# Performance work log

Measured on AMD Instinct MI355X. Metric: run time of the kernel, lower is better.

The kernel has to match this reference:

```python
import jax, jax.numpy as jnp
import numpy as np

EDGE_TYPES = 5
D = 256      # input_dim == output_dim
HID = 128    # hard-coded hidden size of agg MLPs


def setup_inputs() -> dict:
    key = jax.random.key(0)
    ks = jax.random.split(key, 8)
    B, E, N = 4, 8000, 2000
    edge_distribution = jax.random.uniform(ks[0], (B, E, EDGE_TYPES), dtype=jnp.float32)
    H = jax.random.normal(ks[1], (B, E, N), dtype=jnp.float32)
    ori = jax.random.normal(ks[2], (B, N, D), dtype=jnp.float32)
    # Stacked per-edge-type MLP params: Linear(D->128), ReLU, Linear(128->D)
    W1 = jax.random.normal(ks[3], (EDGE_TYPES, D, HID), dtype=jnp.float32) * (1.0 / np.sqrt(D))
    b1 = jax.random.normal(ks[4], (EDGE_TYPES, HID), dtype=jnp.float32) * 0.01
    W2 = jax.random.normal(ks[5], (EDGE_TYPES, HID, D), dtype=jnp.float32) * (1.0 / np.sqrt(HID))
    b2 = jax.random.normal(ks[6], (EDGE_TYPES, D), dtype=jnp.float32) * 0.01
    return {"edge_distribution": edge_distribution, "H": H, "ori": ori,
            "W1": W1, "b1": b1, "W2": W2, "b2": b2}


def reference(edge_distribution, H, ori, W1, b1, W2, b2):
    # edges = H @ ori : [B, E, D]
    edges = jnp.matmul(H, ori)
    # Per-edge-type 2-layer MLP, vectorized over the type axis t
    h = jax.nn.relu(jnp.einsum('bed,tdh->tbeh', edges, W1) + b1[:, None, None, :])  # [T,B,E,HID]
    mlp_out = jnp.einsum('tbeh,thd->tbed', h, W2) + b2[:, None, None, :]            # [T,B,E,D]
    # Gated accumulate: sum_t edge_distribution[...,t] * mlp_out[t]
    edge_feature = jnp.einsum('bet,tbed->bed', edge_distribution, mlp_out)          # [B,E,D]
    # node_feature = concat(H^T @ edge_feature, ori)
    node_feature = jnp.concatenate(
        [jnp.matmul(jnp.swapaxes(H, 1, 2), edge_feature), ori], axis=-1)            # [B,N,2D]
    return node_feature
```

## Files before the change

### kernel.cpp

```cpp
#include <hip/hip_runtime.h>

typedef unsigned short u16;
typedef short bf16x8 __attribute__((ext_vector_type(8)));
typedef float f32x4 __attribute__((ext_vector_type(4)));
typedef unsigned short u16x8 __attribute__((ext_vector_type(8)));

#define GLL16(gp, lp) __builtin_amdgcn_global_load_lds( \
    (__attribute__((address_space(1))) const unsigned int*)(gp), \
    (__attribute__((address_space(3))) unsigned int*)(lp), 16, 0, 0)

static __device__ __forceinline__ u16 f2bf(float f){
  unsigned u = __builtin_bit_cast(unsigned, f);
  u += 0x7fffu + ((u >> 16) & 1u);
  return (u16)(u >> 16);
}

__global__ __launch_bounds__(256) void prep_ht(const float* __restrict__ H, u16* __restrict__ HT){
  __shared__ u16 t[64*68];
  const int b = blockIdx.z;
  const int e0 = blockIdx.x*64, n0 = blockIdx.y*64;
  const float* Hb = H + (size_t)b*8000*2000;
  u16* To = HT + (size_t)b*2048*8000;
  const int tid = threadIdx.x;
  const int cg = (tid&15)*4, rb = tid>>4;
  #pragma unroll
  for (int rr=0; rr<4; rr++){
    int row = rb + rr*16;
    int gn = n0 + cg;
    float4 v = make_float4(0.f,0.f,0.f,0.f);
    if (gn < 2000) v = *(const float4*)(Hb + (size_t)(e0+row)*2000 + gn);
    ushort4 o; o.x=f2bf(v.x); o.y=f2bf(v.y); o.z=f2bf(v.z); o.w=f2bf(v.w);
    *(ushort4*)(&t[row*68 + cg]) = o;
  }
  __syncthreads();
  const int er8 = (tid&7)*8;
  #pragma unroll
  for (int rr=0; rr<2; rr++){
    int nr = (tid>>3) + rr*32;
    u16x8 v;
    #pragma unroll
    for (int j=0;j<8;j++) v[j] = t[(er8+j)*68 + nr];
    *(u16x8*)(To + (size_t)(n0+nr)*8000 + e0 + er8) = v;
  }
}

__global__ void transpose_f32(const float* __restrict__ src, u16* __restrict__ dst,
                              int R, int C, int Rpad, long sB, long dB){
  __shared__ u16 tile[32][33];
  const int b = blockIdx.z;
  src += (long)b*sB; dst += (long)b*dB;
  const int r0 = blockIdx.x*32, c0 = blockIdx.y*32;
  const int j = threadIdx.x & 31, i0 = threadIdx.x >> 5;
  #pragma unroll
  for (int ii=0; ii<32; ii+=8){
    int r = r0+i0+ii, c = c0+j;
    u16 v = 0;
    if (r < R && c < C) v = f2bf(src[(long)r*C + c]);
    tile[i0+ii][j] = v;
  }
  __syncthreads();
  #pragma unroll
  for (int ii=0; ii<32; ii+=8){
    int c = c0+i0+ii, r = r0+j;
    if (c < C && r < Rpad) dst[(long)c*Rpad + r] = tile[j][i0+ii];
  }
}

__global__ void transpose_u16(const u16* __restrict__ src, u16* __restrict__ dst,
                              int R, int C, int Rpad, long sB, long dB){
  __shared__ u16 tile[32][33];
  const int b = blockIdx.z;
  src += (long)b*sB; dst += (long)b*dB;
  const int r0 = blockIdx.x*32, c0 = blockIdx.y*32;
  const int j = threadIdx.x & 31, i0 = threadIdx.x >> 5;
  #pragma unroll
  for (int ii=0; ii<32; ii+=8){
    int r = r0+i0+ii, c = c0+j;
    u16 v = 0;
    if (r < R && c < C) v = src[(long)r*C + c];
    tile[i0+ii][j] = v;
  }
  __syncthreads();
  #pragma unroll
  for (int ii=0; ii<32; ii+=8){
    int c = c0+i0+ii, r = r0+j;
    if (c < C && r < Rpad) dst[(long)c*Rpad + r] = tile[j][i0+ii];
  }
}

__global__ void ori_copy(const float* __restrict__ ori, float* __restrict__ out){
  int idx = blockIdx.x*256 + threadIdx.x;
  int c4 = (idx & 63)*4;
  int row = idx >> 6;
  float4 v = *(const float4*)(ori + (size_t)row*256 + c4);
  *(float4*)(out + (size_t)row*512 + c4) = make_float4(0.f,0.f,0.f,0.f);
  *(float4*)(out + (size_t)row*512 + 256 + c4) = v;
}

__global__ __launch_bounds__(256,2) void g1_kernel(
    const float* __restrict__ Hm, const u16* __restrict__ oriT, u16* __restrict__ edges){
  __shared__ u16 As[2][128*32];
  __shared__ u16 Bs[2][256*32];
  const int b = blockIdx.y, bm = blockIdx.x*128;
  const int tid = threadIdx.x;
  const int w = tid>>6, quad = (tid&63)>>4, l16 = tid&15;
  const int wm = (w&1)*64, wn = (w>>1)*128;
  const float* Ab = Hm + (size_t)b*8000*2000 + (size_t)bm*2000;
  const u16*  Bb = oriT + (size_t)b*256*2048;

  float4 pa[4];
  auto loadA = [&](int kt){
    const int k0 = kt*32;
    #pragma unroll
    for (int i=0;i<4;i++){
      int idx = i*256+tid, row = idx>>3, c4 = (idx&7)*4;
      bool ok = (bm+row < 8000) && (k0+c4 < 2000);
      pa[i] = ok ? *(const float4*)(Ab + (size_t)row*2000 + k0+c4) : make_float4(0.f,0.f,0.f,0.f);
    }
  };
  auto storeA = [&](int kt){
    const int buf = kt&1;
    #pragma unroll
    for (int i=0;i<4;i++){
      int idx = i*256+tid;
      ushort4 o; o.x=f2bf(pa[i].x); o.y=f2bf(pa[i].y); o.z=f2bf(pa[i].z); o.w=f2bf(pa[i].w);
      *(ushort4*)(&As[buf][idx*4]) = o;
    }
  };
  auto stageB = [&](int kt){
    const int buf = kt&1, k0 = kt*32;
    #pragma unroll
    for (int i=0;i<4;i++){
      int idx = i*256+tid, row = idx>>2, c8 = (idx&3)*8;
      GLL16(Bb + (size_t)row*2048 + k0+c8, &Bs[buf][(i*256 + w*64)*8]);
    }
  };

  f32x4 acc[4][8];
  #pragma unroll
  for (int i=0;i<4;i++)
    #pragma unroll
    for (int j=0;j<8;j++) acc[i][j] = (f32x4){0.f,0.f,0.f,0.f};

  loadA(0); stageB(0);
  for (int kt=0; kt<64; kt++){
    storeA(kt);
    __syncthreads();
    if (kt+1 < 64){ loadA(kt+1); stageB(kt+1); }
    const int buf = kt&1;
    bf16x8 af[4], bf[8];
    #pragma unroll
    for (int mi=0;mi<4;mi++) af[mi] = *(const bf16x8*)(&As[buf][(wm+mi*16+l16)*32 + quad*8]);
    #pragma unroll
    for (int ni=0;ni<8;ni++) bf[ni] = *(const bf16x8*)(&Bs[buf][(wn+ni*16+l16)*32 + quad*8]);
    #pragma unroll
    for (int mi=0;mi<4;mi++)
      #pragma unroll
      for (int ni=0;ni<8;ni++)
        acc[mi][ni] = __builtin_amdgcn_mfma_f32_16x16x32_bf16(af[mi], bf[ni], acc[mi][ni], 0,0,0);
  }
  #pragma unroll
  for (int mi=0;mi<4;mi++){
    #pragma unroll
    for (int r=0;r<4;r++){
      int gm = bm + wm + mi*16 + quad*4 + r;
      if (gm >= 8000) continue;
      u16* dst = edges + ((size_t)b*8000 + gm)*256;
      #pragma unroll
      for (int ni=0;ni<8;ni++) dst[wn + ni*16 + l16] = f2bf(acc[mi][ni][r]);
    }
  }
}

__global__ __launch_bounds__(256,2) void m1_kernel(
    const u16* __restrict__ edges, const u16* __restrict__ W1T,
    const float* __restrict__ b1, const float* __restrict__ edist, u16* __restrict__ H1){
  __shared__ u16 As[2][128*32];
  __shared__ u16 Bs[2][128*32];
  __shared__ float eds[128], b1s[128];
  const int t = blockIdx.y, bm = blockIdx.x*128;
  const int tid = threadIdx.x;
  const int w = tid>>6, quad = (tid&63)>>4, l16 = tid&15;
  const int wm = (w&1)*64, wn = (w>>1)*64;
  if (tid < 128){ eds[tid] = edist[(size_t)(bm+tid)*5 + t]; b1s[tid] = b1[t*128+tid]; }
  const u16* Ab = edges + (size_t)bm*256;
  const u16* Bb = W1T + (size_t)t*128*256;

  auto stage = [&](int kt){
    const int buf = kt&1, k0 = kt*32;
    #pragma unroll
    for (int i=0;i<2;i++){
      int idx = i*256+tid, row = idx>>2, c8 = (idx&3)*8;
      GLL16(Ab + (size_t)row*256 + k0+c8, &As[buf][(i*256 + w*64)*8]);
      GLL16(Bb + (size_t)row*256 + k0+c8, &Bs[buf][(i*256 + w*64)*8]);
    }
  };

  f32x4 acc[4][4];
  #pragma unroll
  for (int i=0;i<4;i++)
    #pragma unroll
    for (int j=0;j<4;j++) acc[i][j] = (f32x4){0.f,0.f,0.f,0.f};

  stage(0);
  for (int kt=0; kt<8; kt++){
    __syncthreads();
    if (kt+1 < 8) stage(kt+1);
    const int buf = kt&1;
    bf16x8 af[4], bf[4];
    #pragma unroll
    for (int mi=0;mi<4;mi++) af[mi] = *(const bf16x8*)(&As[buf][(wm+mi*16+l16)*32 + quad*8]);
    #pragma unroll
    for (int ni=0;ni<4;ni++) bf[ni] = *(const bf16x8*)(&Bs[buf][(wn+ni*16+l16)*32 + quad*8]);
    #pragma unroll
    for (int mi=0;mi<4;mi++)
      #pragma unroll
      for (int ni=0;ni<4;ni++)
        acc[mi][ni] = __builtin_amdgcn_mfma_f32_16x16x32_bf16(af[mi], bf[ni], acc[mi][ni], 0,0,0);
  }
  #pragma unroll
  for (int mi=0;mi<4;mi++){
    #pragma unroll
    for (int r=0;r<4;r++){
      int lrow = wm + mi*16 + quad*4 + r;
      float s = eds[lrow];
      u16* dst = H1 + ((size_t)t*32000 + bm + lrow)*128;
      #pragma unroll
      for (int ni=0;ni<4;ni++){
        int lc = wn + ni*16 + l16;
        float v = fmaxf(acc[mi][ni][r] + b1s[lc], 0.f) * s;
        dst[lc] = f2bf(v);
      }
    }
  }
}

__global__ __launch_bounds__(256,2) void m2_kernel(
    const u16* __restrict__ H1, const u16* __restrict__ W2T,
    const float* __restrict__ b2, const float* __restrict__ edist, u16* __restrict__ EF){
  __shared__ u16 As[2][128*32];
  __shared__ u16 Bs[2][128*32];
  __shared__ float eds[640], b2s[640];
  const int bm = blockIdx.x*128, bn = blockIdx.y*128;
  const int tid = threadIdx.x;
  const int w = tid>>6, quad = (tid&63)>>4, l16 = tid&15;
  const int wm = (w&1)*64, wn = (w>>1)*64;
  for (int i=tid;i<640;i+=256){
    eds[i] = edist[(size_t)bm*5 + i];
    b2s[i] = b2[(i>>7)*256 + bn + (i&127)];
  }
  auto stage = [&](int kt){
    const int buf = kt&1, t = kt>>2, k0 = (kt&3)*32;
    #pragma unroll
    for (int i=0;i<2;i++){
      int idx = i*256+tid, row = idx>>2, c8 = (idx&3)*8;
      GLL16(H1 + ((size_t)t*32000 + bm+row)*128 + k0+c8, &As[buf][(i*256 + w*64)*8]);
      GLL16(W2T + ((size_t)t*256 + bn+row)*128 + k0+c8, &Bs[buf][(i*256 + w*64)*8]);
    }
  };

  f32x4 acc[4][4];
  #pragma unroll
  for (int i=0;i<4;i++)
    #pragma unroll
    for (int j=0;j<4;j++) acc[i][j] = (f32x4){0.f,0.f,0.f,0.f};

  stage(0);
  for (int kt=0; kt<20; kt++){
    __syncthreads();
    if (kt+1 < 20) stage(kt+1);
    const int buf = kt&1;
    bf16x8 af[4], bf[4];
    #pragma unroll
    for (int mi=0;mi<4;mi++) af[mi] = *(const bf16x8*)(&As[buf][(wm+mi*16+l16)*32 + quad*8]);
    #pragma unroll
    for (int ni=0;ni<4;ni++) bf[ni] = *(const bf16x8*)(&Bs[buf][(wn+ni*16+l16)*32 + quad*8]);
    #pragma unroll
    for (int mi=0;mi<4;mi++)
      #pragma unroll
      for (int ni=0;ni<4;ni++)
        acc[mi][ni] = __builtin_amdgcn_mfma_f32_16x16x32_bf16(af[mi], bf[ni], acc[mi][ni], 0,0,0);
  }
  #pragma unroll
  for (int mi=0;mi<4;mi++){
    #pragma unroll
    for (int r=0;r<4;r++){
      int lrow = wm + mi*16 + quad*4 + r;
      float e0=eds[lrow*5+0], e1=eds[lrow*5+1], e2=eds[lrow*5+2], e3=eds[lrow*5+3], e4=eds[lrow*5+4];
      u16* dst = EF + (size_t)(bm+lrow)*256 + bn;
      #pragma unroll
      for (int ni=0;ni<4;ni++){
        int lc = wn + ni*16 + l16;
        float bias = e0*b2s[lc] + e1*b2s[128+lc] + e2*b2s[256+lc] + e3*b2s[384+lc] + e4*b2s[512+lc];
        dst[lc] = f2bf(acc[mi][ni][r] + bias);
      }
    }
  }
}

__global__ __launch_bounds__(256,2) void g3_kernel(
    const u16* __restrict__ HT, const u16* __restrict__ EFt, float* __restrict__ out){
  __shared__ u16 As[2][128*32];
  __shared__ u16 Bs[2][256*32];
  const int bm = blockIdx.x*128, ks = blockIdx.y, b = blockIdx.z;
  const int tid = threadIdx.x;
  const int w = tid>>6, quad = (tid&63)>>4, l16 = tid&15;
  const int wm = (w&1)*64, wn = (w>>1)*128;
  const u16* Ab = HT + (size_t)b*2048*8000 + (size_t)bm*8000;
  const u16* Bb = EFt + (size_t)b*256*8000;
  const int it0 = (250*ks)/8, it1 = (250*(ks+1))/8;

  auto stage = [&](int kt){
    const int buf = kt&1, k0 = kt*32;
    #pragma unroll
    for (int i=0;i<2;i++){
      int idx = i*256+tid, row = idx>>2, c8 = (idx&3)*8;
      GLL16(Ab + (size_t)row*8000 + k0+c8, &As[buf][(i*256 + w*64)*8]);
    }
    #pragma unroll
    for (int i=0;i<4;i++){
      int idx = i*256+tid, row = idx>>2, c8 = (idx&3)*8;
      GLL16(Bb + (size_t)row*8000 + k0+c8, &Bs[buf][(i*256 + w*64)*8]);
    }
  };

  f32x4 acc[4][8];
  #pragma unroll
  for (int i=0;i<4;i++)
    #pragma unroll
    for (int j=0;j<8;j++) acc[i][j] = (f32x4){0.f,0.f,0.f,0.f};

  stage(it0);
  for (int kt=it0; kt<it1; kt++){
    __syncthreads();
    if (kt+1 < it1) stage(kt+1);
    const int buf = kt&1;
    bf16x8 af[4], bf[8];
    #pragma unroll
    for (int mi=0;mi<4;mi++) af[mi] = *(const bf16x8*)(&As[buf][(wm+mi*16+l16)*32 + quad*8]);
    #pragma unroll
    for (int ni=0;ni<8;ni++) bf[ni] = *(const bf16x8*)(&Bs[buf][(wn+ni*16+l16)*32 + quad*8]);
    #pragma unroll
    for (int mi=0;mi<4;mi++)
      #pragma unroll
      for (int ni=0;ni<8;ni++)
        acc[mi][ni] = __builtin_amdgcn_mfma_f32_16x16x32_bf16(af[mi], bf[ni], acc[mi][ni], 0,0,0);
  }
  #pragma unroll
  for (int mi=0;mi<4;mi++){
    #pragma unroll
    for (int r=0;r<4;r++){
      int gm = bm + wm + mi*16 + quad*4 + r;
      if (gm >= 2000) continue;
      float* dst = out + ((size_t)b*2000 + gm)*512;
      #pragma unroll
      for (int ni=0;ni<8;ni++) atomicAdd(dst + wn + ni*16 + l16, acc[mi][ni][r]);
    }
  }
}

extern "C" void kernel_launch(void* const* d_in, const int* in_sizes, int n_in,
                              void* d_out, int out_size, void* d_ws, size_t ws_size,
                              hipStream_t stream) {
  const float* ed  = (const float*)d_in[0];
  const float* Hm  = (const float*)d_in[1];
  const float* ori = (const float*)d_in[2];
  const float* W1  = (const float*)d_in[3];
  const float* b1  = (const float*)d_in[4];
  const float* W2  = (const float*)d_in[5];
  const float* b2  = (const float*)d_in[6];
  float* out = (float*)d_out;
  char* ws = (char*)d_ws;

  u16* HT    = (u16*)(ws);
  u16* oriT  = (u16*)(ws + 131072000);
  u16* W1T   = (u16*)(ws + 135266304);
  u16* W2T   = (u16*)(ws + 135593984);
  u16* edges = (u16*)(ws + 135921664);
  u16* H1    = (u16*)(ws + 152305664);
  u16* EF    = (u16*)(ws + 193265664);
  u16* EFt   = edges;

  hipLaunchKernelGGL(prep_ht, dim3(125,32,4), dim3(256), 0, stream, Hm, HT);
  hipLaunchKernelGGL(transpose_f32, dim3(64,8,4), dim3(256), 0, stream,
                     ori, oriT, 2000, 256, 2048, 512000L, 524288L);
  hipLaunchKernelGGL(transpose_f32, dim3(8,4,5), dim3(256), 0, stream,
                     W1, W1T, 256, 128, 256, 32768L, 32768L);
  hipLaunchKernelGGL(transpose_f32, dim3(4,8,5), dim3(256), 0, stream,
                     W2, W2T, 128, 256, 128, 32768L, 32768L);
  hipLaunchKernelGGL(ori_copy, dim3(2000), dim3(256), 0, stream, ori, out);

  hipLaunchKernelGGL(g1_kernel, dim3(63,4), dim3(256), 0, stream, Hm, oriT, edges);
  hipLaunchKernelGGL(m1_kernel, dim3(250,5), dim3(256), 0, stream, edges, W1T, b1, ed, H1);
  hipLaunchKernelGGL(m2_kernel, dim3(250,2), dim3(256), 0, stream, H1, W2T, b2, ed, EF);
  hipLaunchKernelGGL(transpose_u16, dim3(250,8,4), dim3(256), 0, stream,
                     EF, EFt, 8000, 256, 8000, 2048000L, 2048000L);
  hipLaunchKernelGGL(g3_kernel, dim3(16,8,4), dim3(256), 0, stream, HT, EFt, out);

  (void)in_sizes; (void)n_in; (void)ws_size;
}
```

Baseline: 659.8 us.

## Fuse H transpose into g1 and replace g3 atomics with split-K partial reduction

Removes the separate prep_ht pass, which read H in fp32 a second time just to build a bf16 transposed copy. g1 now writes HT from an extra LDS transposed tile while it converts H for its own GEMM. g3 drops from 8 to 4 K-splits and writes plain partial sums to a workspace instead of doing atomics into the output. A new assemble kernel sums the partials and copies ori, which replaces ori_copy. This adds LDS pressure and scattered LDS stores in g1, plus an extra reduction pass over the partials.

```diff
diff --git a/kernel.cpp b/kernel.cpp
--- a/kernel.cpp
+++ b/kernel.cpp
@@ -13,35 +13,6 @@
   unsigned u = __builtin_bit_cast(unsigned, f);
   u += 0x7fffu + ((u >> 16) & 1u);
   return (u16)(u >> 16);
-}
-
-__global__ __launch_bounds__(256) void prep_ht(const float* __restrict__ H, u16* __restrict__ HT){
-  __shared__ u16 t[64*68];
-  const int b = blockIdx.z;
-  const int e0 = blockIdx.x*64, n0 = blockIdx.y*64;
-  const float* Hb = H + (size_t)b*8000*2000;
-  u16* To = HT + (size_t)b*2048*8000;
-  const int tid = threadIdx.x;
-  const int cg = (tid&15)*4, rb = tid>>4;
-  #pragma unroll
-  for (int rr=0; rr<4; rr++){
-    int row = rb + rr*16;
-    int gn = n0 + cg;
-    float4 v = make_float4(0.f,0.f,0.f,0.f);
-    if (gn < 2000) v = *(const float4*)(Hb + (size_t)(e0+row)*2000 + gn);
-    ushort4 o; o.x=f2bf(v.x); o.y=f2bf(v.y); o.z=f2bf(v.z); o.w=f2bf(v.w);
-    *(ushort4*)(&t[row*68 + cg]) = o;
-  }
-  __syncthreads();
-  const int er8 = (tid&7)*8;
-  #pragma unroll
-  for (int rr=0; rr<2; rr++){
-    int nr = (tid>>3) + rr*32;
-    u16x8 v;
-    #pragma unroll
-    for (int j=0;j<8;j++) v[j] = t[(er8+j)*68 + nr];
-    *(u16x8*)(To + (size_t)(n0+nr)*8000 + e0 + er8) = v;
-  }
 }
 
 __global__ void transpose_f32(const float* __restrict__ src, u16* __restrict__ dst,
@@ -88,25 +59,19 @@
   }
 }
 
-__global__ void ori_copy(const float* __restrict__ ori, float* __restrict__ out){
-  int idx = blockIdx.x*256 + threadIdx.x;
-  int c4 = (idx & 63)*4;
-  int row = idx >> 6;
-  float4 v = *(const float4*)(ori + (size_t)row*256 + c4);
-  *(float4*)(out + (size_t)row*512 + c4) = make_float4(0.f,0.f,0.f,0.f);
-  *(float4*)(out + (size_t)row*512 + 256 + c4) = v;
-}
-
 __global__ __launch_bounds__(256,2) void g1_kernel(
-    const float* __restrict__ Hm, const u16* __restrict__ oriT, u16* __restrict__ edges){
+    const float* __restrict__ Hm, const u16* __restrict__ oriT,
+    u16* __restrict__ edges, u16* __restrict__ HT){
   __shared__ u16 As[2][128*32];
   __shared__ u16 Bs[2][256*32];
+  __shared__ u16 At[2][32*136];
   const int b = blockIdx.y, bm = blockIdx.x*128;
   const int tid = threadIdx.x;
   const int w = tid>>6, quad = (tid&63)>>4, l16 = tid&15;
   const int wm = (w&1)*64, wn = (w>>1)*128;
   const float* Ab = Hm + (size_t)b*8000*2000 + (size_t)bm*2000;
   const u16*  Bb = oriT + (size_t)b*256*2048;
+  u16* HTb = HT + (size_t)b*2048*8000;
 
   float4 pa[4];
   auto loadA = [&](int kt){
@@ -122,16 +87,21 @@
     const int buf = kt&1;
     #pragma unroll
     for (int i=0;i<4;i++){
-      int idx = i*256+tid;
+      int idx = i*256+tid, row = idx>>3, c4 = (idx&7)*4;
       ushort4 o; o.x=f2bf(pa[i].x); o.y=f2bf(pa[i].y); o.z=f2bf(pa[i].z); o.w=f2bf(pa[i].w);
       *(ushort4*)(&As[buf][idx*4]) = o;
+      At[buf][(c4+0)*136 + row] = o.x;
+      At[buf][(c4+1)*136 + row] = o.y;
+      At[buf][(c4+2)*136 + row] = o.z;
+      At[buf][(c4+3)*136 + row] = o.w;
     }
   };
   auto stageB = [&](int kt){
     const int buf = kt&1, k0 = kt*32;
     #pragma unroll
     for (int i=0;i<4;i++){
-      int idx = i*256+tid, row = idx>>2, c8 = (idx&3)*8;
+      int idx = i*256+tid;
+      int row = idx>>2, c8 = (idx&3)*8;
       GLL16(Bb + (size_t)row*2048 + k0+c8, &Bs[buf][(i*256 + w*64)*8]);
     }
   };
@@ -147,7 +117,16 @@
     storeA(kt);
     __syncthreads();
     if (kt+1 < 64){ loadA(kt+1); stageB(kt+1); }
-    const int buf = kt&1;
+    const int buf = kt&1, k0 = kt*32;
+    #pragma unroll
+    for (int j2=0;j2<2;j2++){
+      int ci = j2*256 + tid;
+      int kk = ci>>4, c = ci&15, m0 = c*8;
+      if (bm + m0 < 8000){
+        u16x8 v = *(const u16x8*)(&At[buf][kk*136 + m0]);
+        *(u16x8*)(HTb + (size_t)(k0+kk)*8000 + bm + m0) = v;
+      }
+    }
     bf16x8 af[4], bf[8];
     #pragma unroll
     for (int mi=0;mi<4;mi++) af[mi] = *(const bf16x8*)(&As[buf][(wm+mi*16+l16)*32 + quad*8]);
@@ -299,7 +278,7 @@
 }
 
 __global__ __launch_bounds__(256,2) void g3_kernel(
-    const u16* __restrict__ HT, const u16* __restrict__ EFt, float* __restrict__ out){
+    const u16* __restrict__ HT, const u16* __restrict__ EFt, float* __restrict__ part){
   __shared__ u16 As[2][128*32];
   __shared__ u16 Bs[2][256*32];
   const int bm = blockIdx.x*128, ks = blockIdx.y, b = blockIdx.z;
@@ -308,7 +287,7 @@
   const int wm = (w&1)*64, wn = (w>>1)*128;
   const u16* Ab = HT + (size_t)b*2048*8000 + (size_t)bm*8000;
   const u16* Bb = EFt + (size_t)b*256*8000;
-  const int it0 = (250*ks)/8, it1 = (250*(ks+1))/8;
+  const int it0 = (250*ks)/4, it1 = (250*(ks+1))/4;
 
   auto stage = [&](int kt){
     const int buf = kt&1, k0 = kt*32;
@@ -346,17 +325,31 @@
       for (int ni=0;ni<8;ni++)
         acc[mi][ni] = __builtin_amdgcn_mfma_f32_16x16x32_bf16(af[mi], bf[ni], acc[mi][ni], 0,0,0);
   }
+  float* dst0 = part + ((size_t)(b*4 + ks)*2048)*256;
   #pragma unroll
   for (int mi=0;mi<4;mi++){
     #pragma unroll
     for (int r=0;r<4;r++){
       int gm = bm + wm + mi*16 + quad*4 + r;
-      if (gm >= 2000) continue;
-      float* dst = out + ((size_t)b*2000 + gm)*512;
-      #pragma unroll
-      for (int ni=0;ni<8;ni++) atomicAdd(dst + wn + ni*16 + l16, acc[mi][ni][r]);
-    }
-  }
+      float* dst = dst0 + (size_t)gm*256;
+      #pragma unroll
+      for (int ni=0;ni<8;ni++) dst[wn + ni*16 + l16] = acc[mi][ni][r];
+    }
+  }
+}
+
+__global__ void assemble_kernel(const float* __restrict__ part, const float* __restrict__ ori,
+                                float* __restrict__ out){
+  const int b = blockIdx.y;
+  int u = blockIdx.x*256 + threadIdx.x;
+  int n = u>>6, c4 = (u&63)*4;
+  f32x4 s = (f32x4){0.f,0.f,0.f,0.f};
+  #pragma unroll
+  for (int ks=0; ks<4; ks++)
+    s += *(const f32x4*)(part + ((size_t)(b*4+ks)*2048 + n)*256 + c4);
+  float* dst = out + ((size_t)(b*2000+n))*512;
+  *(f32x4*)(dst + c4) = s;
+  *(f32x4*)(dst + 256 + c4) = *(const f32x4*)(ori + ((size_t)(b*2000+n))*256 + c4);
 }
 
 extern "C" void kernel_launch(void* const* d_in, const int* in_sizes, int n_in,
@@ -380,22 +373,22 @@
   u16* H1    = (u16*)(ws + 152305664);
   u16* EF    = (u16*)(ws + 193265664);
   u16* EFt   = edges;
-
-  hipLaunchKernelGGL(prep_ht, dim3(125,32,4), dim3(256), 0, stream, Hm, HT);
+  float* part = (float*)H1;
+
   hipLaunchKernelGGL(transpose_f32, dim3(64,8,4), dim3(256), 0, stream,
                      ori, oriT, 2000, 256, 2048, 512000L, 524288L);
   hipLaunchKernelGGL(transpose_f32, dim3(8,4,5), dim3(256), 0, stream,
                      W1, W1T, 256, 128, 256, 32768L, 32768L);
   hipLaunchKernelGGL(transpose_f32, dim3(4,8,5), dim3(256), 0, stream,
                      W2, W2T, 128, 256, 128, 32768L, 32768L);
-  hipLaunchKernelGGL(ori_copy, dim3(2000), dim3(256), 0, stream, ori, out);
-
-  hipLaunchKernelGGL(g1_kernel, dim3(63,4), dim3(256), 0, stream, Hm, oriT, edges);
+
+  hipLaunchKernelGGL(g1_kernel, dim3(63,4), dim3(256), 0, stream, Hm, oriT, edges, HT);
   hipLaunchKernelGGL(m1_kernel, dim3(250,5), dim3(256), 0, stream, edges, W1T, b1, ed, H1);
   hipLaunchKernelGGL(m2_kernel, dim3(250,2), dim3(256), 0, stream, H1, W2T, b2, ed, EF);
   hipLaunchKernelGGL(transpose_u16, dim3(250,8,4), dim3(256), 0, stream,
                      EF, EFt, 8000, 256, 8000, 2048000L, 2048000L);
-  hipLaunchKernelGGL(g3_kernel, dim3(16,8,4), dim3(256), 0, stream, HT, EFt, out);
+  hipLaunchKernelGGL(g3_kernel, dim3(16,4,4), dim3(256), 0, stream, HT, EFt, part);
+  hipLaunchKernelGGL(assemble_kernel, dim3(500,4), dim3(256), 0, stream, part, ori, out);
 
   (void)in_sizes; (void)n_in; (void)ws_size;
 }
```

Result: faster. 586.4 us (-11.1%).
